# Optimization experiments

Measured on AMD Instinct MI355X. Metric: run time of the kernel, lower is better.

Reference implementation:

```python
import jax, jax.numpy as jnp
import numpy as np

# MatrixVT core: depth softmax -> vertical-weight depth reduction (H collapsed),
# horizontal feature reduction (max over H), then BEV lifting via the MatrixVT
# factorized projection: bev = ((D' @ circle_map) * ray_map)^T @ F'.
# Dims: B=4 batch, N=6 cams, D=112 depth bins, H=16, W=44 feat map, C=80 out
# channels, X=Y=128 BEV grid (x/y_bound [-51.2,51.2,0.8]).

BEV_X, BEV_Y = 128, 128

def conv2d_same(x, w, b):
    # x: [N,C,H,W], w: [O,I,3,3]
    y = jax.lax.conv_general_dilated(x, w, window_strides=(1, 1), padding='SAME',
                                     dimension_numbers=('NCHW', 'OIHW', 'NCHW'))
    return y + b[None, :, None, None]

def setup_inputs() -> dict:
    key = jax.random.key(0)
    ks = jax.random.split(key, 8)
    B, N, C, D, H, W = 4, 6, 80, 112, 16, 44
    XY = BEV_X * BEV_Y
    return {
        'feature': jax.random.normal(ks[0], (B * N, C, H, W), jnp.float32),
        'depth_logits': jax.random.normal(ks[1], (B * N, D, H, W), jnp.float32),
        'circle_map': jax.random.uniform(ks[2], (B, D, XY), jnp.float32),
        'ray_map': jax.random.uniform(ks[3], (B, N * W, XY), jnp.float32),
        'vw_w1': jax.random.normal(ks[4], (64, C, 3, 3), jnp.float32) * 0.05,
        'vw_b1': jnp.zeros((64,), jnp.float32),
        'vw_w2': jax.random.normal(ks[5], (1, 64, 3, 3), jnp.float32) * 0.05,
        'vw_b2': jnp.zeros((1,), jnp.float32),
    }

def reference(feature, depth_logits, circle_map, ray_map, vw_w1, vw_b1, vw_w2, vw_b2):
    # depth distribution over the D bins (DepthNet softmax)
    depth = jax.nn.softmax(depth_logits, axis=1)                      # [BN,D,H,W]
    # DepthReducer: vertical weighter (conv-relu-conv, softmax over H)
    h = jax.nn.relu(conv2d_same(feature, vw_w1, vw_b1))
    vert_w = jax.nn.softmax(conv2d_same(h, vw_w2, vw_b2), axis=2)     # [BN,1,H,W]
    depth_prime = jnp.sum(depth * vert_w, axis=2)                     # [BN,D,W]
    # HoriConv reduction: collapse H by max
    feat_prime = jnp.max(feature, axis=2)                             # [BN,C,W]
    B = circle_map.shape[0]
    D = depth_prime.shape[1]
    C = feat_prime.shape[1]
    depth_p = depth_prime.transpose(0, 2, 1).reshape(B, -1, D)        # [B, N*W, D]
    feat_p = feat_prime.transpose(0, 2, 1).reshape(B, -1, C)          # [B, N*W, C]
    # MatrixVT factorized projection
    proj = jnp.einsum('bkd,bdv->bkv', depth_p, circle_map) * ray_map  # [B, N*W, XY]
    bev = jnp.einsum('bkv,bkc->bvc', proj, feat_p)                    # [B, XY, C]
    return bev.transpose(0, 2, 1).reshape(B, C, BEV_X, BEV_Y)
```

## Files before the change

kernel.cpp:

```cpp
#include <hip/hip_runtime.h>
#include <hip/hip_bf16.h>

#define BN 24
#define BATCH 4
#define NCAM 6
#define CF 80
#define C2 64
#define DD 112
#define HH 16
#define WW 44
#define KTOT 264
#define KPAD 288
#define DPAD 128
#define XY 16384
#define VT 64
#define KC 96
#define CIP 96

typedef __bf16 bf16x8 __attribute__((ext_vector_type(8)));
typedef float f32x4 __attribute__((ext_vector_type(4)));

__global__ __launch_bounds__(256) void k0_prepack(const float* __restrict__ w1,
                                                  __bf16* __restrict__ wpk) {
    int e = blockIdx.x * 256 + threadIdx.x;
    if (e >= 9 * C2 * CIP) return;
    int kk = e / (C2 * CIP);
    int r  = e % (C2 * CIP);
    int co = r / CIP;
    int ci = r % CIP;
    float v = 0.f;
    if (ci < CF) v = w1[((co * CF + ci) * 3 + kk / 3) * 3 + kk % 3];
    wpk[e] = (__bf16)v;
}

__global__ __launch_bounds__(256) void k1_conv1(const float* __restrict__ feat,
                                                const __bf16* __restrict__ wpk,
                                                const float* __restrict__ b1,
                                                float* __restrict__ hbuf) {
    int bn = blockIdx.x >> 3;
    int hq = blockIdx.x & 7;
    int h0 = hq * 2;
    __shared__ __bf16 fsl[5][48][CIP];
    __shared__ __bf16 wlds[C2][CIP];
    int t = threadIdx.x;

    uint4 zz = make_uint4(0, 0, 0, 0);
    uint4* fz = (uint4*)&fsl[0][0][0];
    for (int e = t; e < 5 * 48 * CIP * 2 / 16; e += 256) fz[e] = zz;
    __syncthreads();
    for (int e = t; e < CF * 4 * WW; e += 256) {
        int ci = e / (4 * WW);
        int r  = e % (4 * WW);
        int yl = r / WW;
        int w  = r % WW;
        int y = h0 + yl - 1;
        if (y >= 0 && y < HH)
            fsl[yl][w + 1][ci] = (__bf16)feat[((bn * CF + ci) * HH + y) * WW + w];
    }

    int wave = t >> 6, lane = t & 63, r16 = lane & 15, kg4 = lane >> 4;
    int nt = (wave < 2) ? 2 : 1;
    int hlA[2], wA[2];
#pragma unroll
    for (int i = 0; i < 2; ++i) {
        int p = (wave + 4 * i) * 16 + r16;
        hlA[i] = p / WW;
        wA[i]  = p % WW;
    }
    f32x4 acc[2][4];
#pragma unroll
    for (int i = 0; i < 2; ++i)
#pragma unroll
        for (int n = 0; n < 4; ++n) acc[i][n] = (f32x4){0.f, 0.f, 0.f, 0.f};

    for (int kk = 0; kk < 9; ++kk) {
        int ky = kk / 3, kx = kk % 3;
        __syncthreads();
        {
            const uint4* wsrc = (const uint4*)(wpk + kk * C2 * CIP);
            uint4* wdst = (uint4*)&wlds[0][0];
            for (int e = t; e < C2 * CIP / 8; e += 256) wdst[e] = wsrc[e];
        }
        __syncthreads();
#pragma unroll
        for (int ks = 0; ks < 3; ++ks) {
            bf16x8 bf[4];
#pragma unroll
            for (int n = 0; n < 4; ++n)
                bf[n] = *(const bf16x8*)&wlds[n * 16 + r16][ks * 32 + kg4 * 8];
            for (int i = 0; i < nt; ++i) {
                bf16x8 af = *(const bf16x8*)&fsl[hlA[i] + ky][wA[i] + kx][ks * 32 + kg4 * 8];
#pragma unroll
                for (int n = 0; n < 4; ++n)
                    acc[i][n] = __builtin_amdgcn_mfma_f32_16x16x32_bf16(af, bf[n], acc[i][n], 0, 0, 0);
            }
        }
    }

    for (int i = 0; i < nt; ++i) {
        int mt = wave + 4 * i;
#pragma unroll
        for (int n = 0; n < 4; ++n) {
            int co = n * 16 + r16;
            float bias = b1[co];
#pragma unroll
            for (int j = 0; j < 4; ++j) {
                int p = mt * 16 + kg4 * 4 + j;
                if (p < 2 * WW) {
                    int hl = p / WW, w = p % WW;
                    float v = acc[i][n][j] + bias;
                    v = fmaxf(v, 0.f);
                    hbuf[((size_t)(bn * HH + h0 + hl) * WW + w) * C2 + co] = v;
                }
            }
        }
    }
}

__global__ __launch_bounds__(256) void k2a_logits(const float* __restrict__ hbuf,
                                                  const float* __restrict__ w2,
                                                  const float* __restrict__ b2,
                                                  float* __restrict__ lg) {
    int bn = blockIdx.x >> 4;
    int h  = blockIdx.x & 15;
    __shared__ float w2t[9][C2];
    __shared__ float pr[4][WW];
    int t = threadIdx.x;
    for (int e = t; e < 9 * C2; e += 256) {
        int kk = e % 9, ci = e / 9;
        w2t[kk][ci] = w2[ci * 9 + kk];
    }
    __syncthreads();
    int w = t & 63;
    int g = t >> 6;
    float acc = 0.f;
    if (w < WW) {
#pragma unroll
        for (int ky = 0; ky < 3; ++ky) {
            int y = h + ky - 1;
            if (y < 0 || y >= HH) continue;
#pragma unroll
            for (int kx = 0; kx < 3; ++kx) {
                int x = w + kx - 1;
                if (x < 0 || x >= WW) continue;
                const float* hp = hbuf + ((size_t)(bn * HH + y) * WW + x) * C2 + g * 16;
                const float* wp = &w2t[ky * 3 + kx][g * 16];
#pragma unroll
                for (int q = 0; q < 4; ++q) {
                    f32x4 hv = *(const f32x4*)(hp + q * 4);
                    acc += wp[q * 4 + 0] * hv[0] + wp[q * 4 + 1] * hv[1]
                         + wp[q * 4 + 2] * hv[2] + wp[q * 4 + 3] * hv[3];
                }
            }
        }
        pr[g][w] = acc;
    }
    __syncthreads();
    if (t < WW) {
        float s = b2[0] + pr[0][t] + pr[1][t] + pr[2][t] + pr[3][t];
        lg[(bn * HH + h) * WW + t] = s;
    }
}

__global__ __launch_bounds__(64) void k2b_softmaxh(const float* __restrict__ lg,
                                                   float* __restrict__ vw) {
    int bn = blockIdx.x;
    int w  = threadIdx.x;
    if (w >= WW) return;
    float r[HH];
    float m = -1e30f;
#pragma unroll
    for (int h = 0; h < HH; ++h) {
        r[h] = lg[(bn * HH + h) * WW + w];
        m = fmaxf(m, r[h]);
    }
    float s = 0.f;
#pragma unroll
    for (int h = 0; h < HH; ++h) { r[h] = expf(r[h] - m); s += r[h]; }
    float inv = 1.f / s;
#pragma unroll
    for (int h = 0; h < HH; ++h)
        vw[(bn * HH + h) * WW + w] = r[h] * inv;
}

__global__ __launch_bounds__(256) void k3_depth(const float* __restrict__ dl,
                                                const float* __restrict__ vw,
                                                __bf16* __restrict__ dp_g) {
    int bx = blockIdx.x;
    int bn = bx / WW;
    int w  = bx % WW;
    __shared__ float sl[HH][DD];
    int t = threadIdx.x;
    for (int e = t; e < HH * DD; e += 256) {
        int d = e % DD, h = e / DD;
        sl[h][d] = dl[((bn * DD + d) * HH + h) * WW + w];
    }
    __syncthreads();
    int g = t >> 4;
    int l = t & 15;
    float v[7];
#pragma unroll
    for (int j = 0; j < 7; ++j) v[j] = sl[g][l + 16 * j];
    float m = v[0];
#pragma unroll
    for (int j = 1; j < 7; ++j) m = fmaxf(m, v[j]);
#pragma unroll
    for (int mk = 1; mk < 16; mk <<= 1) m = fmaxf(m, __shfl_xor(m, mk, 64));
    float s = 0.f;
#pragma unroll
    for (int j = 0; j < 7; ++j) { v[j] = expf(v[j] - m); s += v[j]; }
#pragma unroll
    for (int mk = 1; mk < 16; mk <<= 1) s += __shfl_xor(s, mk, 64);
    float wv = vw[bn * HH * WW + g * WW + w] / s;
#pragma unroll
    for (int j = 0; j < 7; ++j) sl[g][l + 16 * j] = v[j] * wv;
    __syncthreads();
    if (t < DD) {
        float acc = 0.f;
#pragma unroll
        for (int h = 0; h < HH; ++h) acc += sl[h][t];
        int b = bn / NCAM, n = bn % NCAM;
        int k = n * WW + w;
        dp_g[(size_t)b * (KPAD * DPAD) + k * DPAD + t] = (__bf16)acc;
    }
}

__global__ __launch_bounds__(256) void k4_featmax(const float* __restrict__ feat,
                                                  __bf16* __restrict__ fpT_g) {
    int tid = blockIdx.x * 256 + threadIdx.x;
    if (tid >= BN * CF * WW) return;
    int bn = tid / (CF * WW);
    int r  = tid % (CF * WW);
    int c = r / WW, w = r % WW;
    float m = -1e30f;
    for (int h = 0; h < HH; ++h)
        m = fmaxf(m, feat[((bn * CF + c) * HH + h) * WW + w]);
    int b = bn / NCAM, n = bn % NCAM;
    fpT_g[(size_t)b * (CF * KPAD) + c * KPAD + n * WW + w] = (__bf16)m;
}

__global__ __launch_bounds__(256, 2) void k5_bev(const __bf16* __restrict__ dp_g,
                                                 const __bf16* __restrict__ fpT_g,
                                                 const float* __restrict__ circle,
                                                 const float* __restrict__ ray,
                                                 float* __restrict__ out) {
    int b  = blockIdx.x >> 8;
    int vt = blockIdx.x & 255;
    int v0 = vt * VT;
    __shared__ __align__(16) __bf16 circleT[VT][136];
    __shared__ __align__(16) __bf16 dps[KC][136];
    __shared__ __align__(16) __bf16 plds[VT][104];
    __shared__ __align__(16) __bf16 fts[CF][104];
    int t = threadIdx.x;
    int wv = t >> 6;
    int lane = t & 63;
    int r16 = lane & 15;
    int kg4 = lane >> 4;

    const float* cb = circle + (size_t)b * DD * XY + v0;
    for (int e = t; e < DD * (VT / 4); e += 256) {
        int d = e >> 4, vq = e & 15;
        float4 cv = *(const float4*)&cb[(size_t)d * XY + vq * 4];
        circleT[vq * 4 + 0][d] = (__bf16)cv.x;
        circleT[vq * 4 + 1][d] = (__bf16)cv.y;
        circleT[vq * 4 + 2][d] = (__bf16)cv.z;
        circleT[vq * 4 + 3][d] = (__bf16)cv.w;
    }
    for (int e = t; e < VT * 16; e += 256) {
        int v = e >> 4, d = DD + (e & 15);
        circleT[v][d] = (__bf16)0.f;
    }

    f32x4 acc[5];
#pragma unroll
    for (int n = 0; n < 5; ++n) acc[n] = (f32x4){0.f, 0.f, 0.f, 0.f};

    const __bf16* dpb = dp_g + (size_t)b * (KPAD * DPAD);
    const __bf16* ftb = fpT_g + (size_t)b * (CF * KPAD);
    const float* rayb = ray + (size_t)b * KTOT * XY + v0;
    int vloc = wv * 16 + kg4 * 4;

    for (int cc = 0; cc < 3; ++cc) {
        int k0 = cc * KC;
        __syncthreads();
        for (int e = t; e < KC * 16; e += 256) {
            int kk = e >> 4, dg = e & 15;
            uint4 u = *(const uint4*)(dpb + (size_t)(k0 + kk) * DPAD + dg * 8);
            *(uint4*)&dps[kk][dg * 8] = u;
        }
        for (int e = t; e < CF * 12; e += 256) {
            int c = e / 12, kg = e % 12;
            uint4 u = *(const uint4*)(ftb + (size_t)c * KPAD + k0 + kg * 8);
            *(uint4*)&fts[c][kg * 8] = u;
        }
        __syncthreads();

        f32x4 pc[6];
#pragma unroll
        for (int n = 0; n < 6; ++n) pc[n] = (f32x4){0.f, 0.f, 0.f, 0.f};
#pragma unroll
        for (int ks = 0; ks < 4; ++ks) {
            bf16x8 af = *(const bf16x8*)&circleT[wv * 16 + r16][ks * 32 + kg4 * 8];
#pragma unroll
            for (int n = 0; n < 6; ++n) {
                bf16x8 bfv = *(const bf16x8*)&dps[n * 16 + r16][ks * 32 + kg4 * 8];
                pc[n] = __builtin_amdgcn_mfma_f32_16x16x32_bf16(af, bfv, pc[n], 0, 0, 0);
            }
        }
#pragma unroll
        for (int n = 0; n < 6; ++n) {
            int k = k0 + n * 16 + r16;
            float4 rv = {0.f, 0.f, 0.f, 0.f};
            if (k < KTOT) rv = *(const float4*)&rayb[(size_t)k * XY + vloc];
            float rvv[4] = {rv.x, rv.y, rv.z, rv.w};
#pragma unroll
            for (int j = 0; j < 4; ++j)
                plds[vloc + j][n * 16 + r16] = (__bf16)(pc[n][j] * rvv[j]);
        }
        __syncthreads();

#pragma unroll
        for (int ks = 0; ks < 3; ++ks) {
            bf16x8 a2 = *(const bf16x8*)&plds[wv * 16 + r16][ks * 32 + kg4 * 8];
#pragma unroll
            for (int n = 0; n < 5; ++n) {
                bf16x8 b2v = *(const bf16x8*)&fts[n * 16 + r16][ks * 32 + kg4 * 8];
                acc[n] = __builtin_amdgcn_mfma_f32_16x16x32_bf16(a2, b2v, acc[n], 0, 0, 0);
            }
        }
    }

    float* ob = out + (size_t)b * CF * XY + v0 + vloc;
#pragma unroll
    for (int n = 0; n < 5; ++n) {
        int c = n * 16 + r16;
        *(float4*)&ob[(size_t)c * XY] = *(float4*)&acc[n];
    }
}

extern "C" void kernel_launch(void* const* d_in, const int* in_sizes, int n_in,
                              void* d_out, int out_size, void* d_ws, size_t ws_size,
                              hipStream_t stream) {
    const float* feat   = (const float*)d_in[0];
    const float* dl     = (const float*)d_in[1];
    const float* circle = (const float*)d_in[2];
    const float* ray    = (const float*)d_in[3];
    const float* w1     = (const float*)d_in[4];
    const float* b1     = (const float*)d_in[5];
    const float* w2     = (const float*)d_in[6];
    const float* b2     = (const float*)d_in[7];
    float* out = (float*)d_out;

    __bf16* dp_g  = (__bf16*)d_ws;
    __bf16* fpT_g = dp_g + BATCH * KPAD * DPAD;
    size_t bf16_bytes = (size_t)(BATCH * KPAD * DPAD + BATCH * CF * KPAD) * 2;
    float* hbuf = (float*)((char*)d_ws + bf16_bytes);
    float* lg   = hbuf + (size_t)BN * HH * WW * C2;
    float* vw   = lg + BN * HH * WW;
    __bf16* wpk = (__bf16*)(vw + BN * HH * WW);

    hipMemsetAsync(d_ws, 0, bf16_bytes, stream);
    hipLaunchKernelGGL(k0_prepack, dim3(216), dim3(256), 0, stream, w1, wpk);
    hipLaunchKernelGGL(k1_conv1, dim3(192), dim3(256), 0, stream, feat, wpk, b1, hbuf);
    hipLaunchKernelGGL(k2a_logits, dim3(384), dim3(256), 0, stream, hbuf, w2, b2, lg);
    hipLaunchKernelGGL(k2b_softmaxh, dim3(24), dim3(64), 0, stream, lg, vw);
    hipLaunchKernelGGL(k3_depth, dim3(BN * WW), dim3(256), 0, stream, dl, vw, dp_g);
    hipLaunchKernelGGL(k4_featmax, dim3((BN * CF * WW + 255) / 256), dim3(256), 0, stream, feat, fpT_g);
    hipLaunchKernelGGL(k5_bev, dim3(BATCH * (XY / VT)), dim3(256), 0, stream, dp_g, fpT_g, circle, ray, out);
}
```

Measured before the change: 256.1 us.

## Restructure conv1 and depth softmax kernels for coalesced loads and more blocks

conv1 now runs one block per output row (384 blocks) with float4 feature loads and weights read straight from global in an MFMA-fragment-friendly prepacked layout, dropping the per-tap LDS weight staging and syncs. The depth softmax is split into a per-(bn,h) kernel that reads depth logits with coalesced float4 rows and writes bf16 weighted partials, followed by a separate H-sum kernel. This replaces the old strided per-column gathers of depth_logits. In exchange it adds an extra kernel launch and a bf16 intermediate round trip, which slightly reduces precision.

```diff
diff --git a/kernel.cpp b/kernel.cpp
--- a/kernel.cpp
+++ b/kernel.cpp
@@ -20,6 +20,13 @@
 typedef __bf16 bf16x8 __attribute__((ext_vector_type(8)));
 typedef float f32x4 __attribute__((ext_vector_type(4)));
 
+static __device__ inline unsigned pk2bf(float a, float b) {
+    __bf16 x = (__bf16)a, y = (__bf16)b;
+    unsigned short ux = __builtin_bit_cast(unsigned short, x);
+    unsigned short uy = __builtin_bit_cast(unsigned short, y);
+    return (unsigned)ux | ((unsigned)uy << 16);
+}
+
 __global__ __launch_bounds__(256) void k0_prepack(const float* __restrict__ w1,
                                                   __bf16* __restrict__ wpk) {
     int e = blockIdx.x * 256 + threadIdx.x;
@@ -30,88 +37,72 @@
     int ci = r % CIP;
     float v = 0.f;
     if (ci < CF) v = w1[((co * CF + ci) * 3 + kk / 3) * 3 + kk % 3];
-    wpk[e] = (__bf16)v;
+    int ks = ci >> 5, kg4 = (ci >> 3) & 3, j = ci & 7;
+    wpk[(size_t)((((kk * 3 + ks) * 4 + kg4) * C2 + co) * 8 + j)] = (__bf16)v;
 }
 
 __global__ __launch_bounds__(256) void k1_conv1(const float* __restrict__ feat,
                                                 const __bf16* __restrict__ wpk,
                                                 const float* __restrict__ b1,
                                                 float* __restrict__ hbuf) {
-    int bn = blockIdx.x >> 3;
-    int hq = blockIdx.x & 7;
-    int h0 = hq * 2;
-    __shared__ __bf16 fsl[5][48][CIP];
-    __shared__ __bf16 wlds[C2][CIP];
+    int bn = blockIdx.x >> 4;
+    int h  = blockIdx.x & 15;
+    __shared__ __bf16 fsl[3][52][104];
     int t = threadIdx.x;
 
     uint4 zz = make_uint4(0, 0, 0, 0);
     uint4* fz = (uint4*)&fsl[0][0][0];
-    for (int e = t; e < 5 * 48 * CIP * 2 / 16; e += 256) fz[e] = zz;
-    __syncthreads();
-    for (int e = t; e < CF * 4 * WW; e += 256) {
-        int ci = e / (4 * WW);
-        int r  = e % (4 * WW);
-        int yl = r / WW;
-        int w  = r % WW;
-        int y = h0 + yl - 1;
-        if (y >= 0 && y < HH)
-            fsl[yl][w + 1][ci] = (__bf16)feat[((bn * CF + ci) * HH + y) * WW + w];
-    }
+    for (int e = t; e < 3 * 52 * 104 * 2 / 16; e += 256) fz[e] = zz;
+    __syncthreads();
+    for (int e = t; e < CF * 3 * 11; e += 256) {
+        int ci = e % CF;
+        int r  = e / CF;
+        int yl = r % 3;
+        int q  = r / 3;
+        int y = h + yl - 1;
+        if (y >= 0 && y < HH) {
+            float4 f = *(const float4*)&feat[((bn * CF + ci) * HH + y) * WW + q * 4];
+            fsl[yl][q * 4 + 1][ci] = (__bf16)f.x;
+            fsl[yl][q * 4 + 2][ci] = (__bf16)f.y;
+            fsl[yl][q * 4 + 3][ci] = (__bf16)f.z;
+            fsl[yl][q * 4 + 4][ci] = (__bf16)f.w;
+        }
+    }
+    __syncthreads();
 
     int wave = t >> 6, lane = t & 63, r16 = lane & 15, kg4 = lane >> 4;
-    int nt = (wave < 2) ? 2 : 1;
-    int hlA[2], wA[2];
-#pragma unroll
-    for (int i = 0; i < 2; ++i) {
-        int p = (wave + 4 * i) * 16 + r16;
-        hlA[i] = p / WW;
-        wA[i]  = p % WW;
-    }
-    f32x4 acc[2][4];
-#pragma unroll
-    for (int i = 0; i < 2; ++i)
-#pragma unroll
-        for (int n = 0; n < 4; ++n) acc[i][n] = (f32x4){0.f, 0.f, 0.f, 0.f};
-
-    for (int kk = 0; kk < 9; ++kk) {
-        int ky = kk / 3, kx = kk % 3;
-        __syncthreads();
-        {
-            const uint4* wsrc = (const uint4*)(wpk + kk * C2 * CIP);
-            uint4* wdst = (uint4*)&wlds[0][0];
-            for (int e = t; e < C2 * CIP / 8; e += 256) wdst[e] = wsrc[e];
-        }
-        __syncthreads();
-#pragma unroll
-        for (int ks = 0; ks < 3; ++ks) {
-            bf16x8 bf[4];
-#pragma unroll
-            for (int n = 0; n < 4; ++n)
-                bf[n] = *(const bf16x8*)&wlds[n * 16 + r16][ks * 32 + kg4 * 8];
-            for (int i = 0; i < nt; ++i) {
-                bf16x8 af = *(const bf16x8*)&fsl[hlA[i] + ky][wA[i] + kx][ks * 32 + kg4 * 8];
-#pragma unroll
-                for (int n = 0; n < 4; ++n)
-                    acc[i][n] = __builtin_amdgcn_mfma_f32_16x16x32_bf16(af, bf[n], acc[i][n], 0, 0, 0);
-            }
-        }
-    }
-
-    for (int i = 0; i < nt; ++i) {
-        int mt = wave + 4 * i;
-#pragma unroll
-        for (int n = 0; n < 4; ++n) {
-            int co = n * 16 + r16;
-            float bias = b1[co];
-#pragma unroll
-            for (int j = 0; j < 4; ++j) {
-                int p = mt * 16 + kg4 * 4 + j;
-                if (p < 2 * WW) {
-                    int hl = p / WW, w = p % WW;
-                    float v = acc[i][n][j] + bias;
-                    v = fmaxf(v, 0.f);
-                    hbuf[((size_t)(bn * HH + h0 + hl) * WW + w) * C2 + co] = v;
+    f32x4 acc[3];
+#pragma unroll
+    for (int m = 0; m < 3; ++m) acc[m] = (f32x4){0.f, 0.f, 0.f, 0.f};
+
+#pragma unroll
+    for (int ky = 0; ky < 3; ++ky) {
+#pragma unroll
+        for (int kx = 0; kx < 3; ++kx) {
+            int kk = ky * 3 + kx;
+#pragma unroll
+            for (int ks = 0; ks < 3; ++ks) {
+                bf16x8 bw = *(const bf16x8*)(wpk +
+                    (size_t)((((kk * 3 + ks) * 4 + kg4) * C2 + wave * 16 + r16) * 8));
+#pragma unroll
+                for (int m = 0; m < 3; ++m) {
+                    bf16x8 af = *(const bf16x8*)&fsl[ky][m * 16 + r16 + kx][ks * 32 + kg4 * 8];
+                    acc[m] = __builtin_amdgcn_mfma_f32_16x16x32_bf16(af, bw, acc[m], 0, 0, 0);
                 }
+            }
+        }
+    }
+
+    int co = wave * 16 + r16;
+    float bias = b1[co];
+#pragma unroll
+    for (int m = 0; m < 3; ++m) {
+#pragma unroll
+        for (int j = 0; j < 4; ++j) {
+            int p = m * 16 + kg4 * 4 + j;
+            if (p < WW) {
+                float v = fmaxf(acc[m][j] + bias, 0.f);
+                hbuf[((size_t)(bn * HH + h) * WW + p) * C2 + co] = v;
             }
         }
     }
@@ -183,45 +174,69 @@
         vw[(bn * HH + h) * WW + w] = r[h] * inv;
 }
 
-__global__ __launch_bounds__(256) void k3_depth(const float* __restrict__ dl,
-                                                const float* __restrict__ vw,
+__global__ __launch_bounds__(256) void k3a_depth(const float* __restrict__ dl,
+                                                 const float* __restrict__ vw,
+                                                 __bf16* __restrict__ part) {
+    int bn = blockIdx.x >> 4;
+    int h  = blockIdx.x & 15;
+    __shared__ float slT[WW][117];
+    int t = threadIdx.x;
+    for (int e = t; e < DD * 11; e += 256) {
+        int d = e / 11, q = e % 11;
+        float4 f = *(const float4*)&dl[((size_t)(bn * DD + d) * HH + h) * WW + q * 4];
+        slT[q * 4 + 0][d] = f.x;
+        slT[q * 4 + 1][d] = f.y;
+        slT[q * 4 + 2][d] = f.z;
+        slT[q * 4 + 3][d] = f.w;
+    }
+    __syncthreads();
+    if (t < 4 * WW) {
+        int w = t >> 2, l = t & 3;
+        float v[28];
+#pragma unroll
+        for (int i = 0; i < 28; ++i) v[i] = slT[w][l + 4 * i];
+        float m = v[0];
+#pragma unroll
+        for (int i = 1; i < 28; ++i) m = fmaxf(m, v[i]);
+        m = fmaxf(m, __shfl_xor(m, 1, 64));
+        m = fmaxf(m, __shfl_xor(m, 2, 64));
+        float s = 0.f;
+#pragma unroll
+        for (int i = 0; i < 28; ++i) { v[i] = __expf(v[i] - m); s += v[i]; }
+        s += __shfl_xor(s, 1, 64);
+        s += __shfl_xor(s, 2, 64);
+        float scale = vw[(bn * HH + h) * WW + w] / s;
+#pragma unroll
+        for (int i = 0; i < 28; ++i) slT[w][l + 4 * i] = v[i] * scale;
+    }
+    __syncthreads();
+    __bf16* pb = part + ((size_t)(bn * HH + h) * WW) * DD;
+    for (int e = t; e < WW * 14; e += 256) {
+        int w = e / 14, dg = e % 14;
+        uint4 u;
+        u.x = pk2bf(slT[w][dg * 8 + 0], slT[w][dg * 8 + 1]);
+        u.y = pk2bf(slT[w][dg * 8 + 2], slT[w][dg * 8 + 3]);
+        u.z = pk2bf(slT[w][dg * 8 + 4], slT[w][dg * 8 + 5]);
+        u.w = pk2bf(slT[w][dg * 8 + 6], slT[w][dg * 8 + 7]);
+        *(uint4*)(pb + (size_t)w * DD + dg * 8) = u;
+    }
+}
+
+__global__ __launch_bounds__(256) void k3b_hsum(const __bf16* __restrict__ part,
                                                 __bf16* __restrict__ dp_g) {
-    int bx = blockIdx.x;
-    int bn = bx / WW;
-    int w  = bx % WW;
-    __shared__ float sl[HH][DD];
-    int t = threadIdx.x;
-    for (int e = t; e < HH * DD; e += 256) {
-        int d = e % DD, h = e / DD;
-        sl[h][d] = dl[((bn * DD + d) * HH + h) * WW + w];
-    }
-    __syncthreads();
-    int g = t >> 4;
-    int l = t & 15;
-    float v[7];
-#pragma unroll
-    for (int j = 0; j < 7; ++j) v[j] = sl[g][l + 16 * j];
-    float m = v[0];
-#pragma unroll
-    for (int j = 1; j < 7; ++j) m = fmaxf(m, v[j]);
-#pragma unroll
-    for (int mk = 1; mk < 16; mk <<= 1) m = fmaxf(m, __shfl_xor(m, mk, 64));
-    float s = 0.f;
-#pragma unroll
-    for (int j = 0; j < 7; ++j) { v[j] = expf(v[j] - m); s += v[j]; }
-#pragma unroll
-    for (int mk = 1; mk < 16; mk <<= 1) s += __shfl_xor(s, mk, 64);
-    float wv = vw[bn * HH * WW + g * WW + w] / s;
-#pragma unroll
-    for (int j = 0; j < 7; ++j) sl[g][l + 16 * j] = v[j] * wv;
-    __syncthreads();
-    if (t < DD) {
+    int bn = blockIdx.x >> 2;
+    int wq = blockIdx.x & 3;
+    int b = bn / NCAM, n = bn % NCAM;
+    int t = threadIdx.x;
+    for (int e = t; e < 11 * DD; e += 256) {
+        int w = wq * 11 + e / DD;
+        int d = e % DD;
         float acc = 0.f;
 #pragma unroll
-        for (int h = 0; h < HH; ++h) acc += sl[h][t];
-        int b = bn / NCAM, n = bn % NCAM;
+        for (int h = 0; h < HH; ++h)
+            acc += (float)part[((size_t)(bn * HH + h) * WW + w) * DD + d];
         int k = n * WW + w;
-        dp_g[(size_t)b * (KPAD * DPAD) + k * DPAD + t] = (__bf16)acc;
+        dp_g[(size_t)(b * KPAD + k) * DPAD + d] = (__bf16)acc;
     }
 }
 
@@ -358,13 +373,15 @@
     float* lg   = hbuf + (size_t)BN * HH * WW * C2;
     float* vw   = lg + BN * HH * WW;
     __bf16* wpk = (__bf16*)(vw + BN * HH * WW);
+    __bf16* part = wpk + 9 * C2 * CIP;
 
     hipMemsetAsync(d_ws, 0, bf16_bytes, stream);
     hipLaunchKernelGGL(k0_prepack, dim3(216), dim3(256), 0, stream, w1, wpk);
-    hipLaunchKernelGGL(k1_conv1, dim3(192), dim3(256), 0, stream, feat, wpk, b1, hbuf);
+    hipLaunchKernelGGL(k1_conv1, dim3(384), dim3(256), 0, stream, feat, wpk, b1, hbuf);
     hipLaunchKernelGGL(k2a_logits, dim3(384), dim3(256), 0, stream, hbuf, w2, b2, lg);
     hipLaunchKernelGGL(k2b_softmaxh, dim3(24), dim3(64), 0, stream, lg, vw);
-    hipLaunchKernelGGL(k3_depth, dim3(BN * WW), dim3(256), 0, stream, dl, vw, dp_g);
+    hipLaunchKernelGGL(k3a_depth, dim3(384), dim3(256), 0, stream, dl, vw, part);
+    hipLaunchKernelGGL(k3b_hsum, dim3(96), dim3(256), 0, stream, part, dp_g);
     hipLaunchKernelGGL(k4_featmax, dim3((BN * CF * WW + 255) / 256), dim3(256), 0, stream, feat, fpT_g);
     hipLaunchKernelGGL(k5_bev, dim3(BATCH * (XY / VT)), dim3(256), 0, stream, dp_g, fpT_g, circle, ray, out);
 }
```

Result: faster. 208.4 us (-18.6%).
